# Performance work log

Measured on AMD Instinct MI355X. Metric: run time of the kernel, lower is better.

## Reference

```python
import jax, jax.numpy as jnp
import numpy as np
from jax import lax

EPS = 1e-8
DN = ('NCHW', 'OIHW', 'NCHW')


def setup_inputs() -> dict:
    key = jax.random.key(0)
    k1, k2 = jax.random.split(key)
    inputs = jax.random.normal(k1, (16, 3, 512, 512), dtype=jnp.float32)
    template = jax.random.normal(k2, (16, 3, 21, 21), dtype=jnp.float32)
    return {"inputs": inputs, "template": template}


def _normalize_template(template):
    # Z-normalize each (batch, channel) plane independently, then divide by
    # patch element count (matches NCC.__init__).
    B, C, th, tw = template.shape
    t = template.reshape(B, C, th * tw)
    t = t - jnp.mean(t, axis=-1, keepdims=True)
    t = t / (jnp.std(t, axis=-1, keepdims=True) + EPS)  # ddof=0 == unbiased=False
    return t.reshape(B, C, th, tw) / (th * tw)


def reference(inputs, template):
    B, C, H, W = inputs.shape
    th, tw = template.shape[2], template.shape[3]
    nt = _normalize_template(template)

    # Per-(b,c) depthwise cross-correlation (the grouped conv with eye-masked
    # weights is exactly a depthwise conv with per-sample filters).
    x = inputs.reshape(1, B * C, H, W)
    w = nt.reshape(B * C, 1, th, tw)
    res = lax.conv_general_dilated(x, w, (1, 1), 'VALID',
                                   dimension_numbers=DN,
                                   feature_group_count=B * C)
    res = res.reshape(B, C, res.shape[2], res.shape[3])  # (B,C,Hout,Wout)

    # Local (patch) std per channel via box filter (shared across batch).
    box = jnp.full((C, 1, th, tw), 1.0 / (th * tw), dtype=inputs.dtype)
    mean = lax.conv_general_dilated(inputs, box, (1, 1), 'VALID',
                                    dimension_numbers=DN, feature_group_count=C)
    mean_sq = lax.conv_general_dilated(inputs * inputs, box, (1, 1), 'VALID',
                                       dimension_numbers=DN, feature_group_count=C)
    std = jnp.sqrt(mean_sq - mean * mean + EPS)

    return res / (std + EPS)
```

## Files before the change

kernel.cpp:

```cpp
#include <hip/hip_runtime.h>
#include <math.h>

typedef __attribute__((ext_vector_type(8)))  short short8;
typedef __attribute__((ext_vector_type(16))) float f32x16;

#define NPLANE 48
#define H 512
#define W 512
#define TH 21
#define OH 492
#define OW 492
#define EPSF 1e-8f

#define STRIDE 168
#define SEG_ROWS 84

#define BONES_HOFF (4128768u / 2)

__device__ inline unsigned short f2bf(float f) {
    unsigned u = __float_as_uint(f);
    return (unsigned short)((u + 0x7FFFu + ((u >> 16) & 1u)) >> 16);
}
__device__ inline float bf2f(unsigned s) {
    return __uint_as_float(s << 16);
}

__global__ void build_b_kernel(const float* __restrict__ tpl,
                               unsigned short* __restrict__ ws16) {
    __shared__ float sm[2];
    const int plane = blockIdx.x;
    const float* t = tpl + plane * 441;
    const int tid = threadIdx.x;
    if (tid < 64) {
        float s = 0.f, s2 = 0.f;
        for (int k = tid; k < 441; k += 64) {
            float x = t[k];
            s += x; s2 += x * x;
        }
#pragma unroll
        for (int o = 32; o >= 1; o >>= 1) {
            s  += __shfl_down(s, o);
            s2 += __shfl_down(s2, o);
        }
        if (tid == 0) {
            float mean = s / 441.f;
            float var = fmaxf(s2 / 441.f - mean * mean, 0.f);
            sm[0] = mean;
            sm[1] = 1.f / ((sqrtf(var) + EPSF) * 441.f);
        }
    }
    __syncthreads();
    const float mean = sm[0], scale = sm[1];

    unsigned short* bc = ws16 + (size_t)plane * 43008;
    for (int i = tid; i < 43008; i += 256) {
        int j = i & 7, lane = (i >> 3) & 63, s = (i >> 9) & 3, u = i >> 11;
        int k = ((lane >> 5) << 3) + j, n = lane & 31;
        int v = 16 * s + k - n;
        float val = (v >= 0 && v < TH) ? (t[u * 21 + v] - mean) * scale : 0.f;
        bc[i] = f2bf(val);
    }
    if (plane == 0) {
        unsigned short* bo = ws16 + BONES_HOFF;
        const unsigned short one = f2bf(1.f);
        for (int i = tid; i < 2048; i += 256) {
            int j = i & 7, lane = (i >> 3) & 63, s = (i >> 9) & 3;
            int k = ((lane >> 5) << 3) + j, n = lane & 31;
            int v = 16 * s + k - n;
            bo[i] = (v >= 0 && v < TH) ? one : (unsigned short)0;
        }
    }
}

__global__ __launch_bounds__(256, 3) void ncc_fused_kernel(
    const float* __restrict__ in, const unsigned short* __restrict__ ws16,
    float* __restrict__ out) {
    __shared__ short seg[SEG_ROWS * STRIDE];
    __shared__ short vbuf[64 * STRIDE];

    const int plane = blockIdx.z;
    const int x0 = blockIdx.x * 128;
    const int y0 = blockIdx.y * 64;
    const int tid = threadIdx.x;
    const int lane = tid & 63;
    const int tr = (tid >> 6) & 1;
    const int tc = tid >> 7;
    const float* src = in + (size_t)plane * H * W;

    for (int i = tid; i < SEG_ROWS * 20; i += 256) {
        int row = i / 20, s8 = i - row * 20;
        int gy = y0 + row, gx = x0 + s8 * 8;
        short8 val;
        if (gy < H && gx + 7 < W) {
            float4 a = *(const float4*)(src + gy * W + gx);
            float4 b = *(const float4*)(src + gy * W + gx + 4);
            val[0] = (short)f2bf(a.x); val[1] = (short)f2bf(a.y);
            val[2] = (short)f2bf(a.z); val[3] = (short)f2bf(a.w);
            val[4] = (short)f2bf(b.x); val[5] = (short)f2bf(b.y);
            val[6] = (short)f2bf(b.z); val[7] = (short)f2bf(b.w);
        } else {
#pragma unroll
            for (int e = 0; e < 8; ++e) {
                float xv = (gy < H && gx + e < W) ? src[gy * W + gx + e] : 0.f;
                val[e] = (short)f2bf(xv);
            }
        }
        *(short8*)&seg[row * STRIDE + s8 * 8] = val;
    }
    __syncthreads();

    const int m = lane & 31;
    const int half = lane >> 5;
    const int abase = (tr * 32 + m) * STRIDE + tc * 64 + half * 8;
    const unsigned short* bc = ws16 + (size_t)plane * 43008 + lane * 8;

    f32x16 acc[2];
#pragma unroll
    for (int t = 0; t < 2; ++t)
#pragma unroll
        for (int e = 0; e < 16; ++e) acc[t][e] = 0.f;

    short8 bf[4], bfn[4];
#pragma unroll
    for (int s = 0; s < 4; ++s)
        bf[s] = *(const short8*)(bc + s * 512);

    for (int u = 0; u < TH; ++u) {
        const int un = (u + 1 < TH) ? u + 1 : 0;
#pragma unroll
        for (int s = 0; s < 4; ++s)
            bfn[s] = *(const short8*)(bc + (un * 4 + s) * 512);

        short8 af[6];
#pragma unroll
        for (int g = 0; g < 6; ++g)
            af[g] = *(const short8*)&seg[abase + u * STRIDE + g * 16];

#pragma unroll
        for (int t = 0; t < 2; ++t) {
#pragma unroll
            for (int s = 0; s < 4; ++s)
                acc[t] = __builtin_amdgcn_mfma_f32_32x32x16_bf16(
                    af[2 * t + s], bf[s], acc[t], 0, 0, 0);
        }
#pragma unroll
        for (int s = 0; s < 4; ++s) bf[s] = bfn[s];
    }

    const unsigned short* bo16 = ws16 + BONES_HOFF + lane * 8;
    short8 bones[4];
#pragma unroll
    for (int s = 0; s < 4; ++s)
        bones[s] = *(const short8*)(bo16 + s * 512);

    if (tid < 160) {
        const int hr = (tid >= 80) ? 32 : 0;
        const int c2 = (tid % 80) * 2;
        float s0 = 0.f, s1 = 0.f;
#pragma unroll
        for (int r = 0; r < 20; ++r) {
            unsigned p = *(const unsigned*)&seg[(hr + r) * STRIDE + c2];
            s0 += bf2f(p & 0xffffu);
            s1 += bf2f(p >> 16);
        }
        for (int y = hr; y < hr + 32; ++y) {
            unsigned p = *(const unsigned*)&seg[(y + 20) * STRIDE + c2];
            s0 += bf2f(p & 0xffffu);
            s1 += bf2f(p >> 16);
            *(unsigned*)&vbuf[y * STRIDE + c2] =
                (unsigned)f2bf(s0) | ((unsigned)f2bf(s1) << 16);
            unsigned q = *(const unsigned*)&seg[y * STRIDE + c2];
            s0 -= bf2f(q & 0xffffu);
            s1 -= bf2f(q >> 16);
        }
    }
    __syncthreads();

    f32x16 aS[2];
#pragma unroll
    for (int t = 0; t < 2; ++t) {
#pragma unroll
        for (int e = 0; e < 16; ++e) aS[t][e] = 0.f;
#pragma unroll
        for (int s = 0; s < 4; ++s) {
            short8 vf = *(const short8*)&vbuf[abase + (2 * t + s) * 16];
            aS[t] = __builtin_amdgcn_mfma_f32_32x32x16_bf16(vf, bones[s],
                                                            aS[t], 0, 0, 0);
        }
    }
    __syncthreads();

    if (tid < 160) {
        const int hr = (tid >= 80) ? 32 : 0;
        const int c2 = (tid % 80) * 2;
        float s0 = 0.f, s1 = 0.f;
#pragma unroll
        for (int r = 0; r < 20; ++r) {
            unsigned p = *(const unsigned*)&seg[(hr + r) * STRIDE + c2];
            float a = bf2f(p & 0xffffu), b = bf2f(p >> 16);
            s0 = fmaf(a, a, s0);
            s1 = fmaf(b, b, s1);
        }
        for (int y = hr; y < hr + 32; ++y) {
            unsigned p = *(const unsigned*)&seg[(y + 20) * STRIDE + c2];
            float a = bf2f(p & 0xffffu), b = bf2f(p >> 16);
            s0 = fmaf(a, a, s0);
            s1 = fmaf(b, b, s1);
            *(unsigned*)&vbuf[y * STRIDE + c2] =
                (unsigned)f2bf(s0) | ((unsigned)f2bf(s1) << 16);
            unsigned q = *(const unsigned*)&seg[y * STRIDE + c2];
            float c = bf2f(q & 0xffffu), d = bf2f(q >> 16);
            s0 = fmaf(-c, c, s0);
            s1 = fmaf(-d, d, s1);
        }
    }
    __syncthreads();

    const float invn = 1.f / 441.f;
    float* outp = out + (size_t)plane * OH * OW;
#pragma unroll
    for (int t = 0; t < 2; ++t) {
        f32x16 aQ;
#pragma unroll
        for (int e = 0; e < 16; ++e) aQ[e] = 0.f;
#pragma unroll
        for (int s = 0; s < 4; ++s) {
            short8 qf = *(const short8*)&vbuf[abase + (2 * t + s) * 16];
            aQ = __builtin_amdgcn_mfma_f32_32x32x16_bf16(qf, bones[s], aQ,
                                                         0, 0, 0);
        }
        const int gx = x0 + tc * 64 + t * 32 + (lane & 31);
        if (gx < OW) {
#pragma unroll
            for (int r = 0; r < 16; ++r) {
                int gy = y0 + tr * 32 + (r & 3) + ((r >> 2) << 3) + half * 4;
                if (gy < OH) {
                    float mean = aS[t][r] * invn;
                    float msq = aQ[r] * invn;
                    float sd = sqrtf(msq - mean * mean + EPSF);
                    outp[(size_t)gy * OW + gx] = acc[t][r] / (sd + EPSF);
                }
            }
        }
    }
}

extern "C" void kernel_launch(void* const* d_in, const int* in_sizes, int n_in,
                              void* d_out, int out_size, void* d_ws,
                              size_t ws_size, hipStream_t stream) {
    const float* inputs = (const float*)d_in[0];
    const float* tmpl = (const float*)d_in[1];
    float* out = (float*)d_out;
    unsigned short* ws16 = (unsigned short*)d_ws;

    build_b_kernel<<<NPLANE, 256, 0, stream>>>(tmpl, ws16);
    ncc_fused_kernel<<<dim3(4, 8, NPLANE), 256, 0, stream>>>(inputs, ws16, out);
}
```

Measured before the change: 164.1 us.

## Fuse box-sum and box-square passes, reuse seg buffer, use packed bf16 convert

Merges the two vertical sliding-window passes (sum and sum of squares) into one pass run by 80 threads over all 64 rows. The squared sums are written back in place into the consumed seg rows, which removes one barrier-separated phase and lets both horizontal MFMA reductions run together. It also fully unrolls the template loop, dropping the manual B-fragment prefetch, and uses the packed bf16 conversion builtin when available. The epilogue switches to fast sqrt and reciprocal intrinsics. In exchange the serial vertical scan runs on fewer threads over twice as many rows, and the fast math intrinsics may lose a little precision.

```diff
diff --git a/kernel.cpp b/kernel.cpp
--- a/kernel.cpp
+++ b/kernel.cpp
@@ -24,6 +24,24 @@
 __device__ inline float bf2f(unsigned s) {
     return __uint_as_float(s << 16);
 }
+
+#if defined(__has_builtin)
+#if __has_builtin(__builtin_amdgcn_cvt_pk_bf16_f32)
+#define HAVE_CVT_PK_BF16 1
+#endif
+#endif
+
+#ifdef HAVE_CVT_PK_BF16
+typedef __attribute__((ext_vector_type(2))) __bf16 bf16x2;
+__device__ inline unsigned pack2bf(float a, float b) {
+    bf16x2 r = __builtin_amdgcn_cvt_pk_bf16_f32(a, b);
+    return *(unsigned*)&r;
+}
+#else
+__device__ inline unsigned pack2bf(float a, float b) {
+    return (unsigned)f2bf(a) | ((unsigned)f2bf(b) << 16);
+}
+#endif
 
 __global__ void build_b_kernel(const float* __restrict__ tpl,
                                unsigned short* __restrict__ ws16) {
@@ -90,22 +108,24 @@
     for (int i = tid; i < SEG_ROWS * 20; i += 256) {
         int row = i / 20, s8 = i - row * 20;
         int gy = y0 + row, gx = x0 + s8 * 8;
-        short8 val;
         if (gy < H && gx + 7 < W) {
             float4 a = *(const float4*)(src + gy * W + gx);
             float4 b = *(const float4*)(src + gy * W + gx + 4);
-            val[0] = (short)f2bf(a.x); val[1] = (short)f2bf(a.y);
-            val[2] = (short)f2bf(a.z); val[3] = (short)f2bf(a.w);
-            val[4] = (short)f2bf(b.x); val[5] = (short)f2bf(b.y);
-            val[6] = (short)f2bf(b.z); val[7] = (short)f2bf(b.w);
+            int4 p;
+            p.x = (int)pack2bf(a.x, a.y);
+            p.y = (int)pack2bf(a.z, a.w);
+            p.z = (int)pack2bf(b.x, b.y);
+            p.w = (int)pack2bf(b.z, b.w);
+            *(int4*)&seg[row * STRIDE + s8 * 8] = p;
         } else {
+            short8 val;
 #pragma unroll
             for (int e = 0; e < 8; ++e) {
                 float xv = (gy < H && gx + e < W) ? src[gy * W + gx + e] : 0.f;
                 val[e] = (short)f2bf(xv);
             }
-        }
-        *(short8*)&seg[row * STRIDE + s8 * 8] = val;
+            *(short8*)&seg[row * STRIDE + s8 * 8] = val;
+        }
     }
     __syncthreads();
 
@@ -114,118 +134,75 @@
     const int abase = (tr * 32 + m) * STRIDE + tc * 64 + half * 8;
     const unsigned short* bc = ws16 + (size_t)plane * 43008 + lane * 8;
 
+    const unsigned short* bo16 = ws16 + BONES_HOFF + lane * 8;
+    short8 bones[4];
+#pragma unroll
+    for (int s = 0; s < 4; ++s)
+        bones[s] = *(const short8*)(bo16 + s * 512);
+
     f32x16 acc[2];
 #pragma unroll
     for (int t = 0; t < 2; ++t)
 #pragma unroll
         for (int e = 0; e < 16; ++e) acc[t][e] = 0.f;
 
-    short8 bf[4], bfn[4];
-#pragma unroll
-    for (int s = 0; s < 4; ++s)
-        bf[s] = *(const short8*)(bc + s * 512);
-
+#pragma unroll
     for (int u = 0; u < TH; ++u) {
-        const int un = (u + 1 < TH) ? u + 1 : 0;
+        short8 bf[4];
 #pragma unroll
         for (int s = 0; s < 4; ++s)
-            bfn[s] = *(const short8*)(bc + (un * 4 + s) * 512);
-
+            bf[s] = *(const short8*)(bc + (u * 4 + s) * 512);
         short8 af[6];
 #pragma unroll
         for (int g = 0; g < 6; ++g)
             af[g] = *(const short8*)&seg[abase + u * STRIDE + g * 16];
-
-#pragma unroll
-        for (int t = 0; t < 2; ++t) {
+#pragma unroll
+        for (int t = 0; t < 2; ++t)
 #pragma unroll
             for (int s = 0; s < 4; ++s)
                 acc[t] = __builtin_amdgcn_mfma_f32_32x32x16_bf16(
                     af[2 * t + s], bf[s], acc[t], 0, 0, 0);
-        }
-#pragma unroll
-        for (int s = 0; s < 4; ++s) bf[s] = bfn[s];
-    }
-
-    const unsigned short* bo16 = ws16 + BONES_HOFF + lane * 8;
-    short8 bones[4];
-#pragma unroll
-    for (int s = 0; s < 4; ++s)
-        bones[s] = *(const short8*)(bo16 + s * 512);
-
-    if (tid < 160) {
-        const int hr = (tid >= 80) ? 32 : 0;
-        const int c2 = (tid % 80) * 2;
-        float s0 = 0.f, s1 = 0.f;
+    }
+    __syncthreads();
+
+    if (tid < 80) {
+        const int c2 = tid * 2;
+        float s0 = 0.f, s1 = 0.f, q0 = 0.f, q1 = 0.f;
 #pragma unroll
         for (int r = 0; r < 20; ++r) {
-            unsigned p = *(const unsigned*)&seg[(hr + r) * STRIDE + c2];
-            s0 += bf2f(p & 0xffffu);
-            s1 += bf2f(p >> 16);
-        }
-        for (int y = hr; y < hr + 32; ++y) {
+            unsigned p = *(const unsigned*)&seg[r * STRIDE + c2];
+            float a = bf2f(p & 0xffffu), b = bf2f(p >> 16);
+            s0 += a; s1 += b;
+            q0 = fmaf(a, a, q0); q1 = fmaf(b, b, q1);
+        }
+        for (int y = 0; y < 64; ++y) {
             unsigned p = *(const unsigned*)&seg[(y + 20) * STRIDE + c2];
-            s0 += bf2f(p & 0xffffu);
-            s1 += bf2f(p >> 16);
-            *(unsigned*)&vbuf[y * STRIDE + c2] =
-                (unsigned)f2bf(s0) | ((unsigned)f2bf(s1) << 16);
-            unsigned q = *(const unsigned*)&seg[y * STRIDE + c2];
-            s0 -= bf2f(q & 0xffffu);
-            s1 -= bf2f(q >> 16);
-        }
-    }
-    __syncthreads();
-
-    f32x16 aS[2];
+            float a = bf2f(p & 0xffffu), b = bf2f(p >> 16);
+            s0 += a; s1 += b;
+            q0 = fmaf(a, a, q0); q1 = fmaf(b, b, q1);
+            *(unsigned*)&vbuf[y * STRIDE + c2] = pack2bf(s0, s1);
+            unsigned o = *(const unsigned*)&seg[y * STRIDE + c2];
+            float c = bf2f(o & 0xffffu), d = bf2f(o >> 16);
+            *(unsigned*)&seg[y * STRIDE + c2] = pack2bf(q0, q1);
+            s0 -= c; s1 -= d;
+            q0 = fmaf(-c, c, q0); q1 = fmaf(-d, d, q1);
+        }
+    }
+    __syncthreads();
+
+    const float invn = 1.f / 441.f;
+    float* outp = out + (size_t)plane * OH * OW;
 #pragma unroll
     for (int t = 0; t < 2; ++t) {
-#pragma unroll
-        for (int e = 0; e < 16; ++e) aS[t][e] = 0.f;
+        f32x16 aS, aQ;
+#pragma unroll
+        for (int e = 0; e < 16; ++e) { aS[e] = 0.f; aQ[e] = 0.f; }
 #pragma unroll
         for (int s = 0; s < 4; ++s) {
             short8 vf = *(const short8*)&vbuf[abase + (2 * t + s) * 16];
-            aS[t] = __builtin_amdgcn_mfma_f32_32x32x16_bf16(vf, bones[s],
-                                                            aS[t], 0, 0, 0);
-        }
-    }
-    __syncthreads();
-
-    if (tid < 160) {
-        const int hr = (tid >= 80) ? 32 : 0;
-        const int c2 = (tid % 80) * 2;
-        float s0 = 0.f, s1 = 0.f;
-#pragma unroll
-        for (int r = 0; r < 20; ++r) {
-            unsigned p = *(const unsigned*)&seg[(hr + r) * STRIDE + c2];
-            float a = bf2f(p & 0xffffu), b = bf2f(p >> 16);
-            s0 = fmaf(a, a, s0);
-            s1 = fmaf(b, b, s1);
-        }
-        for (int y = hr; y < hr + 32; ++y) {
-            unsigned p = *(const unsigned*)&seg[(y + 20) * STRIDE + c2];
-            float a = bf2f(p & 0xffffu), b = bf2f(p >> 16);
-            s0 = fmaf(a, a, s0);
-            s1 = fmaf(b, b, s1);
-            *(unsigned*)&vbuf[y * STRIDE + c2] =
-                (unsigned)f2bf(s0) | ((unsigned)f2bf(s1) << 16);
-            unsigned q = *(const unsigned*)&seg[y * STRIDE + c2];
-            float c = bf2f(q & 0xffffu), d = bf2f(q >> 16);
-            s0 = fmaf(-c, c, s0);
-            s1 = fmaf(-d, d, s1);
-        }
-    }
-    __syncthreads();
-
-    const float invn = 1.f / 441.f;
-    float* outp = out + (size_t)plane * OH * OW;
-#pragma unroll
-    for (int t = 0; t < 2; ++t) {
-        f32x16 aQ;
-#pragma unroll
-        for (int e = 0; e < 16; ++e) aQ[e] = 0.f;
-#pragma unroll
-        for (int s = 0; s < 4; ++s) {
-            short8 qf = *(const short8*)&vbuf[abase + (2 * t + s) * 16];
+            aS = __builtin_amdgcn_mfma_f32_32x32x16_bf16(vf, bones[s], aS,
+                                                         0, 0, 0);
+            short8 qf = *(const short8*)&seg[abase + (2 * t + s) * 16];
             aQ = __builtin_amdgcn_mfma_f32_32x32x16_bf16(qf, bones[s], aQ,
                                                          0, 0, 0);
         }
@@ -235,10 +212,12 @@
             for (int r = 0; r < 16; ++r) {
                 int gy = y0 + tr * 32 + (r & 3) + ((r >> 2) << 3) + half * 4;
                 if (gy < OH) {
-                    float mean = aS[t][r] * invn;
+                    float mean = aS[r] * invn;
                     float msq = aQ[r] * invn;
-                    float sd = sqrtf(msq - mean * mean + EPSF);
-                    outp[(size_t)gy * OW + gx] = acc[t][r] / (sd + EPSF);
+                    float sd =
+                        __builtin_amdgcn_sqrtf(msq - mean * mean + EPSF);
+                    outp[(size_t)gy * OW + gx] =
+                        acc[t][r] * __builtin_amdgcn_rcpf(sd + EPSF);
                 }
             }
         }
```

Result: no change. 164.1 us (+0.0%).
